# Performance work log

Measured on AMD Instinct MI355X. Metric: run time of the kernel, lower is better.

## Reference

```python
import jax, jax.numpy as jnp
import numpy as np

N, E, T = 20000, 320000, 64
INP, EMB, OUT = 128, 16, 3
HEADS, MSIZE, MDIM, KDIM, VDIM = 4, 1024, 128, 64, 64


def setup_inputs() -> dict:
    key = jax.random.key(0)
    ks = iter(jax.random.split(key, 64))

    def nrm(shape, s=0.05):
        return jax.random.normal(next(ks), shape, dtype=jnp.float32) * s

    return dict(
        x=jax.random.normal(next(ks), (N, INP), dtype=jnp.float32),
        edge_index=jax.random.randint(next(ks), (2, E), 0, N),
        index=5,
        inp_types=jax.random.randint(next(ks), (T,), 0, 4),
        log_return=jax.random.normal(next(ks), (T,), dtype=jnp.float32),
        # SAGEConv 1 (SoftmaxAggregation temp t1, lin_l/lin_r, bias=False)
        t1=jnp.ones((1, INP), jnp.float32),
        W1l=nrm((INP, 512)), W1r=nrm((INP, 512)),
        ln1g_w=jnp.ones((512,), jnp.float32), ln1g_b=jnp.zeros((512,), jnp.float32),
        # SAGEConv 2
        t2=jnp.ones((1, 512), jnp.float32),
        W2l=nrm((512, 256)), W2r=nrm((512, 256)),
        ln2g_w=jnp.ones((256,), jnp.float32), ln2g_b=jnp.zeros((256,), jnp.float32),
        # MemPooling(256,128,heads=4,num_clusters=1)
        mp_k=nrm((HEADS, 1, 256), 1.0),
        mp_conv=nrm((HEADS,), 0.5),            # Conv2d(heads,1,1,bias=False)
        mp_lin=nrm((256, 128)),                # Linear(in,out,bias=False)
        fxg_w=nrm((128, 256)), fxg_b=jnp.zeros((256,), jnp.float32),
        # PolicyNet head
        emb=nrm((4, EMB), 1.0),
        fk_w=nrm((256, KDIM)), fk_b=jnp.zeros((KDIM,), jnp.float32),
        fv_w=nrm((256, VDIM)), fv_b=jnp.zeros((VDIM,), jnp.float32),
        # MultiHeadMemory
        mem=nrm((HEADS, MSIZE, MDIM), 1.0),
        mfk_w=nrm((MDIM, KDIM)), mfk_b=jnp.zeros((KDIM,), jnp.float32),
        mfv_w=nrm((MDIM, VDIM)), mfv_b=jnp.zeros((VDIM,), jnp.float32),
        mfx_w=nrm((VDIM * HEADS, VDIM)), mfx_b=jnp.zeros((VDIM,), jnp.float32),
        f1_w=nrm((INP + EMB + 2 * VDIM + 1, 512)),
        n1_w=jnp.ones((512,), jnp.float32), n1_b=jnp.zeros((512,), jnp.float32),
        f2_w=nrm((512, 256)),
        n2_w=jnp.ones((256,), jnp.float32), n2_b=jnp.zeros((256,), jnp.float32),
        f3_w=nrm((256, OUT)), f3_b=jnp.zeros((OUT,), jnp.float32),
    )


def _forward(x, t1, W1l, W1r, ln1g_w, ln1g_b, t2, W2l, W2r, ln2g_w, ln2g_b,
             mp_k, mp_conv, mp_lin, fxg_w, fxg_b, emb, fk_w, fk_b, fv_w, fv_b,
             mem, mfk_w, mfk_b, mfv_w, mfv_b, mfx_w, mfx_b,
             f1_w, n1_w, n1_b, f2_w, n2_w, n2_b, f3_w, f3_b,
             log_return, edge_index, inp_types, index):
    n = x.shape[0]
    src, dst = edge_index[0], edge_index[1]

    def sage(h, t, Wl, Wr):
        hj = h[src]                                    # [E, C] gather
        gate = hj * t                                  # learned softmax temperature
        m = jax.ops.segment_max(gate, dst, num_segments=n)
        e = jnp.exp(gate - m[dst])                     # segment-stable softmax
        s = jax.ops.segment_sum(e, dst, num_segments=n)
        agg = jax.ops.segment_sum(hj * (e / s[dst]), dst, num_segments=n)
        return agg @ Wl + h @ Wr                       # SAGEConv, bias=False

    def graph_ln(h, w, b, eps=1e-5):                   # PyG LayerNorm, mode='graph'
        hc = h - jnp.mean(h)
        return hc / jnp.sqrt(jnp.mean(hc * hc) + eps) * w + b

    h = jax.nn.relu(graph_ln(sage(x, t1, W1l, W1r), ln1g_w, ln1g_b))
    h = jax.nn.relu(graph_ln(sage(h, t2, W2l, W2r), ln2g_w, ln2g_b))

    # MemPooling (single graph => B=1), tau=1: student-t kernel over sq. distances
    H, K, C = mp_k.shape
    kk = mp_k.reshape(H * K, C)
    d2 = jnp.maximum(jnp.sum(kk * kk, 1)[:, None] - 2.0 * (kk @ h.T)
                     + jnp.sum(h * h, 1)[None, :], 0.0)        # [H*K, N]
    dist = 1.0 / (1.0 + d2)
    dist = dist.reshape(H, K, n).transpose(0, 2, 1)[None]      # [1, H, N, K]
    S = dist / jnp.sum(dist, -1, keepdims=True)
    S = jax.nn.softmax(jnp.einsum('h,bhnk->bnk', mp_conv, S), axis=-1)  # [1, N, K]
    zp = jnp.einsum('bnk,nc->bkc', S, h)[:, 0, :]              # squeeze(1), K==1
    z = (zp @ mp_lin) @ fxg_w + fxg_b                          # [1, 256]

    q = jax.nn.softmax(z @ fk_w + fk_b, axis=-1)               # [1, key_dim]
    v = z @ fv_w + fv_b                                        # [1, val_dim]

    # MultiHeadMemory
    km = jax.nn.softmax(mem @ mfk_w + mfk_b, axis=-1)          # [H, M, key]
    vm = mem @ mfv_w + mfv_b                                   # [H, M, val]
    w = jax.nn.softmax(jnp.einsum('bk,hnk->bhn', q, km), axis=-1)
    mv = jnp.einsum('bhn,hnv->bhv', w, vm).reshape(q.shape[0], -1)
    m_out = mv @ mfx_w + mfx_b                                 # [1, val]

    zz = jnp.concatenate([v, m_out], axis=-1)                  # [1, 2*val]
    t_len = inp_types.shape[0]
    xi = jnp.broadcast_to(x[index][None, :], (t_len, x.shape[1]))
    zb = jnp.broadcast_to(zz, (t_len, zz.shape[1]))
    feat = jnp.concatenate([xi, emb[inp_types], log_return.reshape(-1, 1), zb], axis=-1)

    def ln(h2, w2, b2, eps=1e-5):                              # nn.LayerNorm (last dim)
        mu = jnp.mean(h2, -1, keepdims=True)
        hc = h2 - mu
        return hc / jnp.sqrt(jnp.mean(hc * hc, -1, keepdims=True) + eps) * w2 + b2

    h1 = jax.nn.relu(ln(feat @ f1_w, n1_w, n1_b))              # dropout = identity (eval)
    h2 = jax.nn.relu(ln(h1 @ f2_w, n2_w, n2_b))
    return jax.nn.softmax(h2 @ f3_w + f3_b, axis=-1)           # [T, out_dim]


def reference(x, edge_index, index, inp_types, log_return, t1, W1l, W1r, ln1g_w, ln1g_b,
              t2, W2l, W2r, ln2g_w, ln2g_b, mp_k, mp_conv, mp_lin, fxg_w, fxg_b, emb,
              fk_w, fk_b, fv_w, fv_b, mem, mfk_w, mfk_b, mfv_w, mfv_b, mfx_w, mfx_b,
              f1_w, n1_w, n1_b, f2_w, n2_w, n2_b, f3_w, f3_b):
    return _forward(x, t1, W1l, W1r, ln1g_w, ln1g_b, t2, W2l, W2r, ln2g_w, ln2g_b,
                    mp_k, mp_conv, mp_lin, fxg_w, fxg_b, emb, fk_w, fk_b, fv_w, fv_b,
                    mem, mfk_w, mfk_b, mfv_w, mfv_b, mfx_w, mfx_b,
                    f1_w, n1_w, n1_b, f2_w, n2_w, n2_b, f3_w, f3_b,
                    log_return, edge_index, inp_types, index)
```

## Files before the change

kernel.cpp:

```cpp
#include <hip/hip_runtime.h>

typedef __attribute__((ext_vector_type(8))) short bf16x8;
typedef __attribute__((ext_vector_type(8))) unsigned short ushort8_t;
typedef __attribute__((ext_vector_type(4))) float f32x4;

__device__ __forceinline__ unsigned short f2bf(float f) {
    unsigned int x = __float_as_uint(f);
    unsigned int r = x + 0x7fffu + ((x >> 16) & 1u);
    return (unsigned short)(r >> 16);
}
__device__ __forceinline__ float bf2f(unsigned short u) {
    return __uint_as_float(((unsigned int)u) << 16);
}
__device__ __forceinline__ void load_lds16(const void* g, void* l) {
    __builtin_amdgcn_global_load_lds((const __attribute__((address_space(1))) void*)g,
                                     (__attribute__((address_space(3))) void*)l, 16, 0, 0);
}

#define LOG2E 1.44269504089f

__global__ void count_kernel(const int* __restrict__ dst, int E, int* __restrict__ counts) {
    int i = blockIdx.x * 256 + threadIdx.x;
    if (i < E) atomicAdd(&counts[dst[i]], 1);
}

template <int CHUNK>
__global__ __launch_bounds__(1024) void scan_kernel(int* __restrict__ cnt,
                                                    int* __restrict__ off, int n) {
    __shared__ int s[1024];
    int tid = threadIdx.x;
    int base = tid * CHUNK;
    int loc[CHUNK];
    int sum = 0;
#pragma unroll
    for (int i = 0; i < CHUNK; ++i) {
        int idx = base + i;
        int v = 0;
        if (idx < n) { v = cnt[idx]; cnt[idx] = 0; }
        sum += v;
        loc[i] = sum;
    }
    s[tid] = sum;
    __syncthreads();
    for (int d = 1; d < 1024; d <<= 1) {
        int t = (tid >= d) ? s[tid - d] : 0;
        __syncthreads();
        s[tid] += t;
        __syncthreads();
    }
    int prev = (tid > 0) ? s[tid - 1] : 0;
    if (tid == 0) off[0] = 0;
#pragma unroll
    for (int i = 0; i < CHUNK; ++i) {
        int idx = base + i;
        if (idx < n) off[idx + 1] = prev + loc[i];
    }
}

__global__ void fill_kernel(const int* __restrict__ src, const int* __restrict__ dst, int E,
                            const int* __restrict__ off, int* __restrict__ cursor,
                            int* __restrict__ srcs) {
    int i = blockIdx.x * 256 + threadIdx.x;
    if (i < E) {
        int d = dst[i];
        int p = atomicAdd(&cursor[d], 1);
        srcs[off[d] + p] = src[i];
    }
}

__global__ __launch_bounds__(256) void cast_bf16(const float* __restrict__ in,
                                                 unsigned short* __restrict__ out, size_t n) {
    size_t stride = (size_t)gridDim.x * 256 * 4;
    for (size_t i = ((size_t)blockIdx.x * 256 + threadIdx.x) * 4; i < n; i += stride) {
        float4 v = *(const float4*)(in + i);
        ushort4 o;
        o.x = f2bf(v.x); o.y = f2bf(v.y); o.z = f2bf(v.z); o.w = f2bf(v.w);
        *(ushort4*)(out + i) = o;
    }
}

__global__ __launch_bounds__(256) void agg512(const unsigned short* __restrict__ h,
                                              const float* __restrict__ t,
                                              const int* __restrict__ off,
                                              const int* __restrict__ srcs,
                                              unsigned short* __restrict__ agg, int n) {
    int wid = threadIdx.x >> 6, lane = threadIdx.x & 63;
    int node = blockIdx.x * 4 + wid;
    if (node >= n) return;
    int beg = off[node], end = off[node + 1];
    int col = lane * 8;
    float tc[8], sE[8], sW[8];
#pragma unroll
    for (int i = 0; i < 8; ++i) { tc[i] = t[col + i] * LOG2E; sE[i] = 0.f; sW[i] = 0.f; }
#define P8(u)                                      \
    _Pragma("unroll") for (int i = 0; i < 8; ++i) { \
        float v = bf2f(u[i]);                       \
        float wv = exp2f(v * tc[i]);                \
        sE[i] += wv; sW[i] += v * wv;               \
    }
    int e = beg;
    for (; e + 4 <= end; e += 4) {
        int s0 = srcs[e], s1 = srcs[e + 1], s2 = srcs[e + 2], s3 = srcs[e + 3];
        ushort8_t u0 = *(const ushort8_t*)(h + (size_t)s0 * 512 + col);
        ushort8_t u1 = *(const ushort8_t*)(h + (size_t)s1 * 512 + col);
        ushort8_t u2 = *(const ushort8_t*)(h + (size_t)s2 * 512 + col);
        ushort8_t u3 = *(const ushort8_t*)(h + (size_t)s3 * 512 + col);
        P8(u0) P8(u1) P8(u2) P8(u3)
    }
    for (; e < end; ++e) {
        int s0 = srcs[e];
        ushort8_t u0 = *(const ushort8_t*)(h + (size_t)s0 * 512 + col);
        P8(u0)
    }
#undef P8
    ushort8_t o;
#pragma unroll
    for (int i = 0; i < 8; ++i) o[i] = f2bf((end > beg) ? (sW[i] / sE[i]) : 0.f);
    *(ushort8_t*)(agg + (size_t)node * 512 + col) = o;
}

__global__ __launch_bounds__(256) void agg128(const unsigned short* __restrict__ h,
                                              const float* __restrict__ t,
                                              const int* __restrict__ off,
                                              const int* __restrict__ srcs,
                                              unsigned short* __restrict__ agg, int n) {
    int wid = threadIdx.x >> 6, lane = threadIdx.x & 63;
    int node = blockIdx.x * 4 + wid;
    if (node >= n) return;
    int beg = off[node], end = off[node + 1];
    int col = lane * 2;
    float t0 = t[col] * LOG2E, t1 = t[col + 1] * LOG2E;
    float e0 = 0.f, e1 = 0.f, w0 = 0.f, w1 = 0.f;
#define P2(u)                                          \
    {                                                  \
        float a = bf2f(u.x), b = bf2f(u.y);            \
        float xa = exp2f(a * t0), xb = exp2f(b * t1);  \
        e0 += xa; e1 += xb; w0 += a * xa; w1 += b * xb; \
    }
    int e = beg;
    for (; e + 8 <= end; e += 8) {
        ushort2 u0 = *(const ushort2*)(h + (size_t)srcs[e] * 128 + col);
        ushort2 u1 = *(const ushort2*)(h + (size_t)srcs[e + 1] * 128 + col);
        ushort2 u2 = *(const ushort2*)(h + (size_t)srcs[e + 2] * 128 + col);
        ushort2 u3 = *(const ushort2*)(h + (size_t)srcs[e + 3] * 128 + col);
        ushort2 u4 = *(const ushort2*)(h + (size_t)srcs[e + 4] * 128 + col);
        ushort2 u5 = *(const ushort2*)(h + (size_t)srcs[e + 5] * 128 + col);
        ushort2 u6 = *(const ushort2*)(h + (size_t)srcs[e + 6] * 128 + col);
        ushort2 u7 = *(const ushort2*)(h + (size_t)srcs[e + 7] * 128 + col);
        P2(u0) P2(u1) P2(u2) P2(u3) P2(u4) P2(u5) P2(u6) P2(u7)
    }
    for (; e < end; ++e) {
        ushort2 u0 = *(const ushort2*)(h + (size_t)srcs[e] * 128 + col);
        P2(u0)
    }
#undef P2
    ushort2 o;
    o.x = f2bf((end > beg) ? (w0 / e0) : 0.f);
    o.y = f2bf((end > beg) ? (w1 / e1) : 0.f);
    *(ushort2*)(agg + (size_t)node * 128 + col) = o;
}

__global__ void pack_w(const float* __restrict__ Wl, const float* __restrict__ Wr,
                       int K1, int K2, int N, unsigned short* __restrict__ Bt) {
    int idx = blockIdx.x * 256 + threadIdx.x;
    int Kc = K1 + K2;
    if (idx < N * Kc) {
        int n = idx / Kc;
        int k = idx - n * Kc;
        float v = (k < K1) ? Wl[(size_t)k * N + n] : Wr[(size_t)(k - K1) * N + n];
        Bt[idx] = f2bf(v);
    }
}

__global__ __launch_bounds__(512) void gemm_dual_mfma2(
    const unsigned short* __restrict__ A1, const unsigned short* __restrict__ A2,
    const unsigned short* __restrict__ Bt,
    unsigned short* __restrict__ Cb, double* __restrict__ part,
    int M, int N, int K1, int K2) {
    const int Kc = K1 + K2;
    __shared__ unsigned short As[128 * 32];
    __shared__ unsigned short Bs[256 * 32];
    __shared__ double rs[512], rs2[512];
    int tid = threadIdx.x;
    int lane = tid & 63, w = tid >> 6;
    int wm = w & 1, wn = w >> 1;
    int m0 = blockIdx.y * 128, n0 = blockIdx.x * 256;
    f32x4 acc[4][4] = {};
    int kg = lane >> 4, lr = lane & 15;
    int ar = tid >> 2, ach = tid & 3;
    int br0 = tid >> 2, bch = tid & 3;

    for (int k0 = 0; k0 < Kc; k0 += 32) {
        const unsigned short* Asrc;
        int kk, Ksrc;
        if (k0 < K1) { Asrc = A1; kk = k0; Ksrc = K1; }
        else         { Asrc = A2; kk = k0 - K1; Ksrc = K2; }
        load_lds16(Asrc + (size_t)(m0 + ar) * Ksrc + kk + ach * 8, &As[tid * 8]);
        load_lds16(Bt + (size_t)(n0 + br0) * Kc + k0 + bch * 8, &Bs[tid * 8]);
        load_lds16(Bt + (size_t)(n0 + 128 + br0) * Kc + k0 + bch * 8, &Bs[(tid + 512) * 8]);
        __syncthreads();
        bf16x8 a[4], b[4];
#pragma unroll
        for (int i = 0; i < 4; ++i)
            a[i] = *(bf16x8*)&As[(wm * 64 + i * 16 + lr) * 32 + kg * 8];
#pragma unroll
        for (int j = 0; j < 4; ++j)
            b[j] = *(bf16x8*)&Bs[(wn * 64 + j * 16 + lr) * 32 + kg * 8];
#pragma unroll
        for (int i = 0; i < 4; ++i)
#pragma unroll
            for (int j = 0; j < 4; ++j)
                acc[i][j] = __builtin_amdgcn_mfma_f32_16x16x32_bf16(a[i], b[j], acc[i][j], 0, 0, 0);
        __syncthreads();
    }
    double s = 0, s2 = 0;
#pragma unroll
    for (int i = 0; i < 4; ++i) {
        int rbase = m0 + wm * 64 + i * 16 + kg * 4;
#pragma unroll
        for (int j = 0; j < 4; ++j) {
            int col = n0 + wn * 64 + j * 16 + lr;
#pragma unroll
            for (int reg = 0; reg < 4; ++reg) {
                int row = rbase + reg;
                if (row < M) {
                    float v = acc[i][j][reg];
                    Cb[(size_t)row * N + col] = f2bf(v);
                    s += v;
                    s2 += (double)v * v;
                }
            }
        }
    }
    rs[tid] = s;
    rs2[tid] = s2;
    __syncthreads();
    for (int d = 256; d; d >>= 1) {
        if (tid < d) { rs[tid] += rs[tid + d]; rs2[tid] += rs2[tid + d]; }
        __syncthreads();
    }
    if (tid == 0) {
        int bid = blockIdx.y * gridDim.x + blockIdx.x;
        part[bid * 2] = rs[0];
        part[bid * 2 + 1] = rs2[0];
    }
}

template <int C>
__global__ __launch_bounds__(256) void ln_relu_ip(unsigned short* __restrict__ z,
                                                  const float* __restrict__ w,
                                                  const float* __restrict__ b,
                                                  const double* __restrict__ part, int nb,
                                                  float invn, size_t n) {
    __shared__ float st[2];
    if (threadIdx.x < 64) {
        double s = 0, s2 = 0;
        for (int i = threadIdx.x; i < nb; i += 64) { s += part[2 * i]; s2 += part[2 * i + 1]; }
        for (int d = 32; d; d >>= 1) { s += __shfl_down(s, d); s2 += __shfl_down(s2, d); }
        if (threadIdx.x == 0) {
            float mu = (float)(s * invn);
            float var = (float)(s2 * invn) - mu * mu;
            st[0] = mu;
            st[1] = rsqrtf(var + 1e-5f);
        }
    }
    __syncthreads();
    float mu = st[0], inv = st[1];
    size_t stride = (size_t)gridDim.x * 256 * 4;
    for (size_t i = ((size_t)blockIdx.x * 256 + threadIdx.x) * 4; i < n; i += stride) {
        ushort4 v = *(const ushort4*)(z + i);
        int c = (int)(i & (C - 1));
        ushort4 o;
        o.x = f2bf(fmaxf((bf2f(v.x) - mu) * inv * w[c] + b[c], 0.f));
        o.y = f2bf(fmaxf((bf2f(v.y) - mu) * inv * w[c + 1] + b[c + 1], 0.f));
        o.z = f2bf(fmaxf((bf2f(v.z) - mu) * inv * w[c + 2] + b[c + 2], 0.f));
        o.w = f2bf(fmaxf((bf2f(v.w) - mu) * inv * w[c + 3] + b[c + 3], 0.f));
        *(ushort4*)(z + i) = o;
    }
}

__global__ __launch_bounds__(256) void colsum_t(const unsigned short* __restrict__ h2,
                                                float* __restrict__ cspartT, int n) {
    __shared__ float red[8 * 256];
    int tid = threadIdx.x;
    int cg = tid & 31;
    int rl = tid >> 5;
    int rows_per = (n + gridDim.x - 1) / gridDim.x;
    int r0 = blockIdx.x * rows_per;
    int r1 = min(n, r0 + rows_per);
    int c8 = cg * 8;
    float acc[8] = {};
    for (int r = r0 + rl; r < r1; r += 8) {
        ushort8_t u = *(const ushort8_t*)(h2 + (size_t)r * 256 + c8);
#pragma unroll
        for (int i = 0; i < 8; ++i) acc[i] += bf2f(u[i]);
    }
#pragma unroll
    for (int i = 0; i < 8; ++i) red[rl * 256 + c8 + i] = acc[i];
    __syncthreads();
    float s = 0;
#pragma unroll
    for (int r = 0; r < 8; ++r) s += red[r * 256 + tid];
    cspartT[tid * 64 + blockIdx.x] = s;
}

__global__ __launch_bounds__(256) void zqv_kernel(const float* __restrict__ cspartT,
                                                  const float* __restrict__ mp_lin,
                                                  const float* __restrict__ fxg_w,
                                                  const float* __restrict__ fxg_b,
                                                  const float* __restrict__ fk_w,
                                                  const float* __restrict__ fk_b,
                                                  const float* __restrict__ fv_w,
                                                  const float* __restrict__ fv_b,
                                                  float* __restrict__ qv) {
    __shared__ float zp_s[256], u_s[128], z_s[256], ql_s[64];
    __shared__ float part_s[1024];
    int tid = threadIdx.x;
    {
        float s = 0;
        const float* p = cspartT + tid * 64;
#pragma unroll
        for (int i = 0; i < 16; ++i) {
            float4 v = *(const float4*)(p + i * 4);
            s += v.x + v.y + v.z + v.w;
        }
        zp_s[tid] = s;
    }
    __syncthreads();
    {
        int og = tid & 31, kc = tid >> 5;
        int j4 = og * 4;
        f32x4 a = {0.f, 0.f, 0.f, 0.f};
        for (int ci = 0; ci < 32; ++ci) {
            int c = kc * 32 + ci;
            float4 w = *(const float4*)(mp_lin + (size_t)c * 128 + j4);
            float zc = zp_s[c];
            a[0] += zc * w.x; a[1] += zc * w.y; a[2] += zc * w.z; a[3] += zc * w.w;
        }
#pragma unroll
        for (int i = 0; i < 4; ++i) part_s[kc * 128 + j4 + i] = a[i];
    }
    __syncthreads();
    if (tid < 128) {
        float s = 0;
#pragma unroll
        for (int kc = 0; kc < 8; ++kc) s += part_s[kc * 128 + tid];
        u_s[tid] = s;
    }
    __syncthreads();
    {
        int og = tid & 63, kc = tid >> 6;
        int j4 = og * 4;
        f32x4 a = {0.f, 0.f, 0.f, 0.f};
        for (int ci = 0; ci < 32; ++ci) {
            int c = kc * 32 + ci;
            float4 w = *(const float4*)(fxg_w + (size_t)c * 256 + j4);
            float uc = u_s[c];
            a[0] += uc * w.x; a[1] += uc * w.y; a[2] += uc * w.z; a[3] += uc * w.w;
        }
#pragma unroll
        for (int i = 0; i < 4; ++i) part_s[kc * 256 + j4 + i] = a[i];
    }
    __syncthreads();
    {
        float s = fxg_b[tid];
#pragma unroll
        for (int kc = 0; kc < 4; ++kc) s += part_s[kc * 256 + tid];
        z_s[tid] = s;
    }
    __syncthreads();
    {
        int og = tid & 15, kc = tid >> 4;
        int j4 = og * 4;
        f32x4 a = {0.f, 0.f, 0.f, 0.f};
        for (int ci = 0; ci < 16; ++ci) {
            int c = kc * 16 + ci;
            float4 w = *(const float4*)(fk_w + (size_t)c * 64 + j4);
            float zc = z_s[c];
            a[0] += zc * w.x; a[1] += zc * w.y; a[2] += zc * w.z; a[3] += zc * w.w;
        }
#pragma unroll
        for (int i = 0; i < 4; ++i) part_s[kc * 64 + j4 + i] = a[i];
    }
    __syncthreads();
    if (tid < 64) {
        float s = fk_b[tid];
#pragma unroll
        for (int kc = 0; kc < 16; ++kc) s += part_s[kc * 64 + tid];
        ql_s[tid] = s;
    }
    __syncthreads();
    {
        int og = tid & 15, kc = tid >> 4;
        int j4 = og * 4;
        f32x4 a = {0.f, 0.f, 0.f, 0.f};
        for (int ci = 0; ci < 16; ++ci) {
            int c = kc * 16 + ci;
            float4 w = *(const float4*)(fv_w + (size_t)c * 64 + j4);
            float zc = z_s[c];
            a[0] += zc * w.x; a[1] += zc * w.y; a[2] += zc * w.z; a[3] += zc * w.w;
        }
#pragma unroll
        for (int i = 0; i < 4; ++i) part_s[kc * 64 + j4 + i] = a[i];
    }
    __syncthreads();
    if (tid < 64) {
        float mx = ql_s[tid];
        for (int d = 32; d; d >>= 1) mx = fmaxf(mx, __shfl_xor(mx, d));
        float e = __expf(ql_s[tid] - mx);
        float s = e;
        for (int d = 32; d; d >>= 1) s += __shfl_xor(s, d);
        qv[tid] = e / s;
        float vv = fv_b[tid];
#pragma unroll
        for (int kc = 0; kc < 16; ++kc) vv += part_s[kc * 64 + tid];
        qv[64 + tid] = vv;
    }
}

__global__ __launch_bounds__(256) void mem_kv_logit(const float* __restrict__ mem,
                                                    const float* __restrict__ mfk_w,
                                                    const float* __restrict__ mfk_b,
                                                    const float* __restrict__ mfv_w,
                                                    const float* __restrict__ mfv_b,
                                                    const float* __restrict__ qv,
                                                    float* __restrict__ logits,
                                                    float* __restrict__ vm) {
    __shared__ float rows[4][128];
    __shared__ float qs[64];
    int tid = threadIdx.x;
    int r0 = blockIdx.x * 4;
    if (tid < 64) qs[tid] = qv[tid];
    for (int i = tid; i < 512; i += 256) rows[i >> 7][i & 127] = mem[(size_t)r0 * 128 + i];
    __syncthreads();
    int lr = tid >> 6;
    int lane = tid & 63;
    const float* row = rows[lr];
    float kl = mfk_b[lane], vl = mfv_b[lane];
#pragma unroll 8
    for (int c = 0; c < 128; ++c) {
        float rv = row[c];
        kl += rv * mfk_w[c * 64 + lane];
        vl += rv * mfv_w[c * 64 + lane];
    }
    float mx = kl;
    for (int d = 32; d; d >>= 1) mx = fmaxf(mx, __shfl_xor(mx, d));
    float e = __expf(kl - mx);
    float s = e;
    for (int d = 32; d; d >>= 1) s += __shfl_xor(s, d);
    float kval = e / s;
    float wl = kval * qs[lane];
    for (int d = 32; d; d >>= 1) wl += __shfl_xor(wl, d);
    size_t gr = (size_t)(r0 + lr);
    if (lane == 0) logits[gr] = wl;
    vm[gr * 64 + lane] = vl;
}

__global__ __launch_bounds__(256) void attend_part(const float* __restrict__ logits,
                                                   const float* __restrict__ vm,
                                                   float* __restrict__ part) {
    int b = blockIdx.x;
    int h = b >> 4;
    int s0 = (b & 15) * 64;
    int tid = threadIdx.x;
    __shared__ float els[64];
    __shared__ float pr[4][64];
    __shared__ float lmax_s, lsum_s;
    if (tid < 64) {
        float lg = logits[h * 1024 + s0 + tid];
        float m = lg;
        for (int d = 32; d; d >>= 1) m = fmaxf(m, __shfl_xor(m, d));
        float e = __expf(lg - m);
        els[tid] = e;
        float s = e;
        for (int d = 32; d; d >>= 1) s += __shfl_xor(s, d);
        if (tid == 0) { lmax_s = m; lsum_s = s; }
    }
    __syncthreads();
    int dd = tid & 63, g = tid >> 6;
    float acc = 0;
    for (int s = g; s < 64; s += 4)
        acc += els[s] * vm[((size_t)h * 1024 + s0 + s) * 64 + dd];
    pr[g][dd] = acc;
    __syncthreads();
    if (tid < 64) {
        float pv = pr[0][tid] + pr[1][tid] + pr[2][tid] + pr[3][tid];
        part[b * 66 + 2 + tid] = pv;
        if (tid == 0) { part[b * 66] = lmax_s; part[b * 66 + 1] = lsum_s; }
    }
}

__global__ __launch_bounds__(256) void attend_final(const float* __restrict__ part,
                                                    const float* __restrict__ mfx_w,
                                                    const float* __restrict__ mfx_b,
                                                    float* __restrict__ m_out) {
    __shared__ float mv[256];
    __shared__ float part_s[1024];
    int tid = threadIdx.x;
    int h = tid >> 6, dd = tid & 63;
    float gmax = -1e30f;
#pragma unroll
    for (int p = 0; p < 16; ++p) gmax = fmaxf(gmax, part[(h * 16 + p) * 66]);
    float total = 0.f, acc = 0.f;
#pragma unroll
    for (int p = 0; p < 16; ++p) {
        float sc = __expf(part[(h * 16 + p) * 66] - gmax);
        total += part[(h * 16 + p) * 66 + 1] * sc;
        acc += part[(h * 16 + p) * 66 + 2 + dd] * sc;
    }
    mv[h * 64 + dd] = acc / total;
    __syncthreads();
    {
        int og = tid & 15, kc = tid >> 4;
        int j4 = og * 4;
        f32x4 a = {0.f, 0.f, 0.f, 0.f};
        for (int ci = 0; ci < 16; ++ci) {
            int c = kc * 16 + ci;
            float4 w = *(const float4*)(mfx_w + (size_t)c * 64 + j4);
            float mc = mv[c];
            a[0] += mc * w.x; a[1] += mc * w.y; a[2] += mc * w.z; a[3] += mc * w.w;
        }
#pragma unroll
        for (int i = 0; i < 4; ++i) part_s[kc * 64 + j4 + i] = a[i];
    }
    __syncthreads();
    if (tid < 64) {
        float s = mfx_b[tid];
#pragma unroll
        for (int kc = 0; kc < 16; ++kc) s += part_s[kc * 64 + tid];
        m_out[tid] = s;
    }
}

__device__ __forceinline__ float block_sum_256(float v, float* red) {
    int tid = threadIdx.x;
    red[tid] = v;
    __syncthreads();
    for (int d = 128; d; d >>= 1) { if (tid < d) red[tid] += red[tid + d]; __syncthreads(); }
    float r = red[0];
    __syncthreads();
    return r;
}

__global__ __launch_bounds__(256) void head_kernel(
    const float* __restrict__ x, const int* __restrict__ index_p,
    const int* __restrict__ inp_types, const float* __restrict__ log_return,
    const float* __restrict__ emb, const float* __restrict__ qv,
    const float* __restrict__ m_out, const float* __restrict__ f1_w,
    const float* __restrict__ n1_w, const float* __restrict__ n1_b,
    const float* __restrict__ f2_w, const float* __restrict__ n2_w,
    const float* __restrict__ n2_b, const float* __restrict__ f3_w,
    const float* __restrict__ f3_b, float* __restrict__ out) {
    __shared__ float feat[273];
    __shared__ float h1[512];
    __shared__ float h2[256];
    __shared__ float red[256];
    __shared__ float l3[3];
    int r = blockIdx.x, tid = threadIdx.x;
    int idx = index_p[0];
    for (int i = tid; i < 273; i += 256) {
        float val;
        if (i < 128) val = x[(size_t)idx * 128 + i];
        else if (i < 144) val = emb[inp_types[r] * 16 + (i - 128)];
        else if (i == 144) val = log_return[r];
        else if (i < 209) val = qv[64 + (i - 145)];
        else val = m_out[i - 209];
        feat[i] = val;
    }
    __syncthreads();
    float a0 = 0, a1 = 0;
    for (int c = 0; c < 273; ++c) {
        float f = feat[c];
        a0 += f * f1_w[c * 512 + tid];
        a1 += f * f1_w[c * 512 + tid + 256];
    }
    float mu = block_sum_256(a0 + a1, red) / 512.f;
    float c0 = a0 - mu, c1 = a1 - mu;
    float var = block_sum_256(c0 * c0 + c1 * c1, red) / 512.f;
    float inv = rsqrtf(var + 1e-5f);
    h1[tid] = fmaxf(c0 * inv * n1_w[tid] + n1_b[tid], 0.f);
    h1[tid + 256] = fmaxf(c1 * inv * n1_w[tid + 256] + n1_b[tid + 256], 0.f);
    __syncthreads();
    float b0 = 0;
    for (int c = 0; c < 512; ++c) b0 += h1[c] * f2_w[c * 256 + tid];
    float mu2 = block_sum_256(b0, red) / 256.f;
    float cc = b0 - mu2;
    float var2 = block_sum_256(cc * cc, red) / 256.f;
    float inv2 = rsqrtf(var2 + 1e-5f);
    h2[tid] = fmaxf(cc * inv2 * n2_w[tid] + n2_b[tid], 0.f);
    __syncthreads();
    if (tid < 3) {
        float a = f3_b[tid];
        for (int c = 0; c < 256; ++c) a += h2[c] * f3_w[c * 3 + tid];
        l3[tid] = a;
    }
    __syncthreads();
    if (tid < 3) {
        float mx = fmaxf(l3[0], fmaxf(l3[1], l3[2]));
        float s = __expf(l3[0] - mx) + __expf(l3[1] - mx) + __expf(l3[2] - mx);
        out[r * 3 + tid] = __expf(l3[tid] - mx) / s;
    }
}

extern "C" void kernel_launch(void* const* d_in, const int* in_sizes, int n_in,
                              void* d_out, int out_size, void* d_ws, size_t ws_size,
                              hipStream_t stream) {
    const float* x = (const float*)d_in[0];
    const int* ei = (const int*)d_in[1];
    const int* index_p = (const int*)d_in[2];
    const int* inp_types = (const int*)d_in[3];
    const float* log_return = (const float*)d_in[4];
    const float* t1 = (const float*)d_in[5];
    const float* W1l = (const float*)d_in[6];
    const float* W1r = (const float*)d_in[7];
    const float* ln1g_w = (const float*)d_in[8];
    const float* ln1g_b = (const float*)d_in[9];
    const float* t2 = (const float*)d_in[10];
    const float* W2l = (const float*)d_in[11];
    const float* W2r = (const float*)d_in[12];
    const float* ln2g_w = (const float*)d_in[13];
    const float* ln2g_b = (const float*)d_in[14];
    const float* mp_lin = (const float*)d_in[17];
    const float* fxg_w = (const float*)d_in[18];
    const float* fxg_b = (const float*)d_in[19];
    const float* emb = (const float*)d_in[20];
    const float* fk_w = (const float*)d_in[21];
    const float* fk_b = (const float*)d_in[22];
    const float* fv_w = (const float*)d_in[23];
    const float* fv_b = (const float*)d_in[24];
    const float* mem = (const float*)d_in[25];
    const float* mfk_w = (const float*)d_in[26];
    const float* mfk_b = (const float*)d_in[27];
    const float* mfv_w = (const float*)d_in[28];
    const float* mfv_b = (const float*)d_in[29];
    const float* mfx_w = (const float*)d_in[30];
    const float* mfx_b = (const float*)d_in[31];
    const float* f1_w = (const float*)d_in[32];
    const float* n1_w = (const float*)d_in[33];
    const float* n1_b = (const float*)d_in[34];
    const float* f2_w = (const float*)d_in[35];
    const float* n2_w = (const float*)d_in[36];
    const float* n2_b = (const float*)d_in[37];
    const float* f3_w = (const float*)d_in[38];
    const float* f3_b = (const float*)d_in[39];
    float* out = (float*)d_out;

    int n = in_sizes[0] / 128;
    int E = in_sizes[1] / 2;
    int T = in_sizes[3];
    const int* src = ei;
    const int* dst = ei + E;

    char* w = (char*)d_ws;
    auto alloc = [&](size_t bytes) {
        char* p = w;
        w += (bytes + 255) & ~(size_t)255;
        return p;
    };
    int* counts = (int*)alloc((size_t)n * 4);
    int* off = (int*)alloc((size_t)(n + 1) * 4);
    int* srcs = (int*)alloc((size_t)E * 4);
    unsigned short* xb = (unsigned short*)alloc((size_t)n * 128 * 2);
    unsigned short* agg1b = (unsigned short*)alloc((size_t)n * 128 * 2);
    unsigned short* z1b = (unsigned short*)alloc((size_t)n * 512 * 2);
    unsigned short* agg2b = (unsigned short*)alloc((size_t)n * 512 * 2);
    unsigned short* z2b = (unsigned short*)alloc((size_t)n * 256 * 2);
    double* partd = (double*)alloc(1024 * 2 * 8);
    float* cspartT = (float*)alloc(256 * 64 * 4);
    float* qv = (float*)alloc(128 * 4);
    float* logits = (float*)alloc((size_t)4 * 1024 * 4);
    float* vm = (float*)alloc((size_t)4 * 1024 * 64 * 4);
    float* apart = (float*)alloc(64 * 66 * 4);
    float* m_out = (float*)alloc(64 * 4);
    unsigned short* Bt1 = (unsigned short*)alloc((size_t)512 * 256 * 2);
    unsigned short* Bt2 = (unsigned short*)alloc((size_t)256 * 1024 * 2);
    alloc(4096);

    int nblk_e = (E + 255) / 256;
    int mblk = (n + 127) / 128;

    hipMemsetAsync(counts, 0, (size_t)n * 4, stream);
    count_kernel<<<nblk_e, 256, 0, stream>>>(dst, E, counts);
    scan_kernel<20><<<1, 1024, 0, stream>>>(counts, off, n);
    fill_kernel<<<nblk_e, 256, 0, stream>>>(src, dst, E, off, counts, srcs);

    pack_w<<<(512 * 256 + 255) / 256, 256, 0, stream>>>(W1l, W1r, 128, 128, 512, Bt1);
    pack_w<<<(256 * 1024 + 255) / 256, 256, 0, stream>>>(W2l, W2r, 512, 512, 256, Bt2);
    cast_bf16<<<1024, 256, 0, stream>>>(x, xb, (size_t)n * 128);

    agg128<<<(n + 3) / 4, 256, 0, stream>>>(xb, t1, off, srcs, agg1b, n);
    gemm_dual_mfma2<<<dim3(2, mblk), 512, 0, stream>>>(agg1b, xb, Bt1, z1b, partd, n, 512, 128, 128);
    ln_relu_ip<512><<<1024, 256, 0, stream>>>(z1b, ln1g_w, ln1g_b, partd, 2 * mblk,
                                              1.0f / ((float)n * 512.f), (size_t)n * 512);

    agg512<<<(n + 3) / 4, 256, 0, stream>>>(z1b, t2, off, srcs, agg2b, n);
    gemm_dual_mfma2<<<dim3(1, mblk), 512, 0, stream>>>(agg2b, z1b, Bt2, z2b, partd, n, 256, 512, 512);
    ln_relu_ip<256><<<512, 256, 0, stream>>>(z2b, ln2g_w, ln2g_b, partd, mblk,
                                             1.0f / ((float)n * 256.f), (size_t)n * 256);

    colsum_t<<<64, 256, 0, stream>>>(z2b, cspartT, n);
    zqv_kernel<<<1, 256, 0, stream>>>(cspartT, mp_lin, fxg_w, fxg_b, fk_w, fk_b, fv_w, fv_b, qv);

    mem_kv_logit<<<1024, 256, 0, stream>>>(mem, mfk_w, mfk_b, mfv_w, mfv_b, qv, logits, vm);
    attend_part<<<64, 256, 0, stream>>>(logits, vm, apart);
    attend_final<<<1, 256, 0, stream>>>(apart, mfx_w, mfx_b, m_out);

    head_kernel<<<T, 256, 0, stream>>>(x, index_p, inp_types, log_return, emb, qv, m_out,
                                       f1_w, n1_w, n1_b, f2_w, n2_w, n2_b, f3_w, f3_b, out);
}
```

Baseline: 318.1 us.

## Pad GEMM LDS tiles, use register loads with bounds, shrink aggregation unroll

The GEMM tile loads move from direct global-to-LDS transfers to ordinary vector loads through registers. They write into LDS rows padded to 40 elements to avoid bank conflicts on the MFMA operand reads, and rows past M are zero-filled, which removes the need for the extra trailing allocation. The softmax aggregation kernels also drop their edge unroll depth (4 to 2 for the 512-wide pass, 8 to 4 for the 128-wide pass), which reduces register pressure but leaves fewer gathers in flight. Staging through registers adds VGPR use and instructions compared with the direct LDS load path.

```diff
diff --git a/kernel.cpp b/kernel.cpp
--- a/kernel.cpp
+++ b/kernel.cpp
@@ -11,10 +11,6 @@
 }
 __device__ __forceinline__ float bf2f(unsigned short u) {
     return __uint_as_float(((unsigned int)u) << 16);
-}
-__device__ __forceinline__ void load_lds16(const void* g, void* l) {
-    __builtin_amdgcn_global_load_lds((const __attribute__((address_space(1))) void*)g,
-                                     (__attribute__((address_space(3))) void*)l, 16, 0, 0);
 }
 
 #define LOG2E 1.44269504089f
@@ -92,22 +88,20 @@
     float tc[8], sE[8], sW[8];
 #pragma unroll
     for (int i = 0; i < 8; ++i) { tc[i] = t[col + i] * LOG2E; sE[i] = 0.f; sW[i] = 0.f; }
-#define P8(u)                                      \
+#define P8(u)                                       \
     _Pragma("unroll") for (int i = 0; i < 8; ++i) { \
         float v = bf2f(u[i]);                       \
         float wv = exp2f(v * tc[i]);                \
         sE[i] += wv; sW[i] += v * wv;               \
     }
     int e = beg;
-    for (; e + 4 <= end; e += 4) {
-        int s0 = srcs[e], s1 = srcs[e + 1], s2 = srcs[e + 2], s3 = srcs[e + 3];
+    for (; e + 2 <= end; e += 2) {
+        int s0 = srcs[e], s1 = srcs[e + 1];
         ushort8_t u0 = *(const ushort8_t*)(h + (size_t)s0 * 512 + col);
         ushort8_t u1 = *(const ushort8_t*)(h + (size_t)s1 * 512 + col);
-        ushort8_t u2 = *(const ushort8_t*)(h + (size_t)s2 * 512 + col);
-        ushort8_t u3 = *(const ushort8_t*)(h + (size_t)s3 * 512 + col);
-        P8(u0) P8(u1) P8(u2) P8(u3)
-    }
-    for (; e < end; ++e) {
+        P8(u0) P8(u1)
+    }
+    if (e < end) {
         int s0 = srcs[e];
         ushort8_t u0 = *(const ushort8_t*)(h + (size_t)s0 * 512 + col);
         P8(u0)
@@ -138,16 +132,12 @@
         e0 += xa; e1 += xb; w0 += a * xa; w1 += b * xb; \
     }
     int e = beg;
-    for (; e + 8 <= end; e += 8) {
+    for (; e + 4 <= end; e += 4) {
         ushort2 u0 = *(const ushort2*)(h + (size_t)srcs[e] * 128 + col);
         ushort2 u1 = *(const ushort2*)(h + (size_t)srcs[e + 1] * 128 + col);
         ushort2 u2 = *(const ushort2*)(h + (size_t)srcs[e + 2] * 128 + col);
         ushort2 u3 = *(const ushort2*)(h + (size_t)srcs[e + 3] * 128 + col);
-        ushort2 u4 = *(const ushort2*)(h + (size_t)srcs[e + 4] * 128 + col);
-        ushort2 u5 = *(const ushort2*)(h + (size_t)srcs[e + 5] * 128 + col);
-        ushort2 u6 = *(const ushort2*)(h + (size_t)srcs[e + 6] * 128 + col);
-        ushort2 u7 = *(const ushort2*)(h + (size_t)srcs[e + 7] * 128 + col);
-        P2(u0) P2(u1) P2(u2) P2(u3) P2(u4) P2(u5) P2(u6) P2(u7)
+        P2(u0) P2(u1) P2(u2) P2(u3)
     }
     for (; e < end; ++e) {
         ushort2 u0 = *(const ushort2*)(h + (size_t)srcs[e] * 128 + col);
@@ -178,8 +168,8 @@
     unsigned short* __restrict__ Cb, double* __restrict__ part,
     int M, int N, int K1, int K2) {
     const int Kc = K1 + K2;
-    __shared__ unsigned short As[128 * 32];
-    __shared__ unsigned short Bs[256 * 32];
+    __shared__ unsigned short As[128 * 40];
+    __shared__ unsigned short Bs[256 * 40];
     __shared__ double rs[512], rs2[512];
     int tid = threadIdx.x;
     int lane = tid & 63, w = tid >> 6;
@@ -187,25 +177,34 @@
     int m0 = blockIdx.y * 128, n0 = blockIdx.x * 256;
     f32x4 acc[4][4] = {};
     int kg = lane >> 4, lr = lane & 15;
-    int ar = tid >> 2, ach = tid & 3;
-    int br0 = tid >> 2, bch = tid & 3;
 
     for (int k0 = 0; k0 < Kc; k0 += 32) {
         const unsigned short* Asrc;
         int kk, Ksrc;
         if (k0 < K1) { Asrc = A1; kk = k0; Ksrc = K1; }
         else         { Asrc = A2; kk = k0 - K1; Ksrc = K2; }
-        load_lds16(Asrc + (size_t)(m0 + ar) * Ksrc + kk + ach * 8, &As[tid * 8]);
-        load_lds16(Bt + (size_t)(n0 + br0) * Kc + k0 + bch * 8, &Bs[tid * 8]);
-        load_lds16(Bt + (size_t)(n0 + 128 + br0) * Kc + k0 + bch * 8, &Bs[(tid + 512) * 8]);
+        {
+            int r = tid >> 2, ch = tid & 3;
+            int gr = m0 + r;
+            ushort8_t v = {0, 0, 0, 0, 0, 0, 0, 0};
+            if (gr < M) v = *(const ushort8_t*)(Asrc + (size_t)gr * Ksrc + kk + ch * 8);
+            *(ushort8_t*)&As[r * 40 + ch * 8] = v;
+        }
+#pragma unroll
+        for (int it = 0; it < 2; ++it) {
+            int idx = tid + it * 512;
+            int r = idx >> 2, ch = idx & 3;
+            const unsigned short* srcp = Bt + (size_t)(n0 + r) * Kc + k0 + ch * 8;
+            *(ushort8_t*)&Bs[r * 40 + ch * 8] = *(const ushort8_t*)srcp;
+        }
         __syncthreads();
         bf16x8 a[4], b[4];
 #pragma unroll
         for (int i = 0; i < 4; ++i)
-            a[i] = *(bf16x8*)&As[(wm * 64 + i * 16 + lr) * 32 + kg * 8];
+            a[i] = *(bf16x8*)&As[(wm * 64 + i * 16 + lr) * 40 + kg * 8];
 #pragma unroll
         for (int j = 0; j < 4; ++j)
-            b[j] = *(bf16x8*)&Bs[(wn * 64 + j * 16 + lr) * 32 + kg * 8];
+            b[j] = *(bf16x8*)&Bs[(wn * 64 + j * 16 + lr) * 40 + kg * 8];
 #pragma unroll
         for (int i = 0; i < 4; ++i)
 #pragma unroll
@@ -674,7 +673,6 @@
     float* m_out = (float*)alloc(64 * 4);
     unsigned short* Bt1 = (unsigned short*)alloc((size_t)512 * 256 * 2);
     unsigned short* Bt2 = (unsigned short*)alloc((size_t)256 * 1024 * 2);
-    alloc(4096);
 
     int nblk_e = (E + 255) / 256;
     int mblk = (n + 127) / 128;
```

New measurement: 317.6 us. About the same (-0.2%).
